# Kernel optimization log

Measured on AMD Instinct MI355X. Metric: run time of the kernel, lower is better.

## Reference

```python
import jax, jax.numpy as jnp
import numpy as np

VOCAB = 50257
EMB = 256
HID = 512
BATCH = 32
SEQ = 512
PAD_ID = 0


def setup_inputs() -> dict:
    key = jax.random.key(0)
    k1, k2, k3, k4, k5, k6 = jax.random.split(key, 6)
    input_ids = jax.random.randint(k1, (BATCH, SEQ), 0, VOCAB, dtype=jnp.int32)
    attention_mask = jax.random.randint(k2, (BATCH, SEQ), 0, 2, dtype=jnp.int32)
    # learned params
    embed_table = jax.random.normal(k3, (VOCAB, EMB), dtype=jnp.float32) * 0.02
    Wx = jax.random.normal(k4, (EMB, HID), dtype=jnp.float32) / np.sqrt(EMB)
    Wh = jax.random.normal(k5, (HID, HID), dtype=jnp.float32) / np.sqrt(HID)
    b = jnp.zeros((HID,), dtype=jnp.float32)
    return {"input_ids": input_ids, "attention_mask": attention_mask,
            "embed_table": embed_table, "Wx": Wx, "Wh": Wh, "b": b}


def reference(input_ids, attention_mask, embed_table, Wx, Wh, b):
    # Embedding lookup: [B, S, E]
    emb = embed_table[input_ids]
    # time-major for scan: [S, B, E] and [S, B]
    xs = jnp.swapaxes(emb, 0, 1)
    ms = jnp.swapaxes(attention_mask, 0, 1)
    h0 = jnp.zeros((emb.shape[0], Wh.shape[0]), dtype=emb.dtype)

    def step(h, xm):
        x_t, m_t = xm  # [B, E], [B]
        h_new = jnp.tanh(x_t @ Wx + h @ Wh + b)  # Elman RNN cell
        h_next = jnp.where((m_t != PAD_ID)[:, None], h_new, h)
        return h_next, h_next

    final_h, all_h_tmajor = jax.lax.scan(step, h0, (xs, ms))
    all_h = jnp.swapaxes(all_h_tmajor, 0, 1)  # [B, S, H]
    return all_h, final_h
```

## Files before the change

### kernel.cpp

```cpp
#include <hip/hip_runtime.h>

#define VOCAB 50257
#define EMB 256
#define HID 512
#define BATCH 32
#define SEQ 512

typedef _Float16 h2 __attribute__((ext_vector_type(2)));
typedef unsigned int u32;

#if __has_builtin(__builtin_amdgcn_fdot2)
#define FDOT2(a, b, c) __builtin_amdgcn_fdot2((a), (b), (c), false)
#else
static __device__ __forceinline__ float FDOT2(h2 a, h2 b, float c) {
    return c + (float)a.x * (float)b.x + (float)a.y * (float)b.y;
}
#endif

#define LBAR() do {                                            \
    asm volatile("s_waitcnt lgkmcnt(0)" ::: "memory");         \
    __builtin_amdgcn_s_barrier();                              \
    asm volatile("" ::: "memory");                             \
} while (0)

static __device__ __forceinline__ h2 mk2(float a, float b) {
    h2 r; r.x = (_Float16)a; r.y = (_Float16)b; return r;
}
static __device__ __forceinline__ u32 pk_rtn(float a, float b) {
    return __builtin_bit_cast(u32, mk2(a, b));
}
static __device__ __forceinline__ h2 as_h2(u32 v) {
    return __builtin_bit_cast(h2, v);
}

__global__ __launch_bounds__(256) void xprec_kernel(
    const int* __restrict__ ids, const float* __restrict__ emb,
    const float* __restrict__ Wx, const float* __restrict__ bias,
    float* __restrict__ allh)
{
    __shared__ float embL[32][EMB];
    const int tid  = threadIdx.x;
    const int tok0 = blockIdx.x * 32;

    {
        const int t    = tid >> 3;
        const int part = tid & 7;
        const int id   = ids[tok0 + t];
        const float4* src = (const float4*)(emb + (size_t)id * EMB + part * 32);
        float4* dst = (float4*)(&embL[t][part * 32]);
#pragma unroll
        for (int k = 0; k < 8; ++k) dst[k] = src[k];
    }
    __syncthreads();

    const int j0 = tid * 2;
    float2 acc[32];
    const float2 bv = *(const float2*)(bias + j0);
#pragma unroll
    for (int t = 0; t < 32; ++t) acc[t] = bv;

    for (int e = 0; e < EMB; e += 4) {
        const float2 w0 = *(const float2*)(Wx + (size_t)(e + 0) * HID + j0);
        const float2 w1 = *(const float2*)(Wx + (size_t)(e + 1) * HID + j0);
        const float2 w2 = *(const float2*)(Wx + (size_t)(e + 2) * HID + j0);
        const float2 w3 = *(const float2*)(Wx + (size_t)(e + 3) * HID + j0);
#pragma unroll
        for (int t = 0; t < 32; ++t) {
            const float4 ev = *(const float4*)(&embL[t][e]);
            acc[t].x += ev.x * w0.x + ev.y * w1.x + ev.z * w2.x + ev.w * w3.x;
            acc[t].y += ev.x * w0.y + ev.y * w1.y + ev.z * w2.y + ev.w * w3.y;
        }
    }

#pragma unroll
    for (int t = 0; t < 32; ++t) {
        *(float2*)(allh + (size_t)(tok0 + t) * HID + j0) = acc[t];
    }
}

__global__ __launch_bounds__(512, 2) void rnn_local_kernel(
    const int* __restrict__ mask, const float* __restrict__ Wh,
    float* __restrict__ allh, float* __restrict__ finalh)
{
    __shared__ uint4 wl[2][8][512];
    __shared__ float zp[8][8][64];
    __shared__ int   mlist[SEQ];
    __shared__ int   nmL;

    const int tid = threadIdx.x;
    const int b   = blockIdx.x;
    const int c   = tid & 63;
    const int p   = tid >> 6;

    int* maskL = (int*)zp;
    maskL[tid] = mask[b * SEQ + tid];
    __syncthreads();
    if (tid == 0) {
        int n = 0;
        for (int t = 0; t < SEQ; ++t) if (maskL[t]) mlist[n++] = t;
        nmL = n;
    }

    const float* wb = Wh + (size_t)(64 * p) * HID + c;
    h2 wv0[32], wv1[32], wv2[32], wv3[32], wv4[32], wv5[32];
#pragma unroll
    for (int i = 0; i < 32; ++i) {
        const float* r0 = wb + (size_t)(2 * i) * HID;
        const float* r1 = r0 + HID;
        wv0[i] = mk2(r0[0 * 64], r1[0 * 64]);
        wv1[i] = mk2(r0[1 * 64], r1[1 * 64]);
        wv2[i] = mk2(r0[2 * 64], r1[2 * 64]);
        wv3[i] = mk2(r0[3 * 64], r1[3 * 64]);
        wv4[i] = mk2(r0[4 * 64], r1[4 * 64]);
        wv5[i] = mk2(r0[5 * 64], r1[5 * 64]);
    }
#pragma unroll
    for (int blk = 0; blk < 8; ++blk) {
        uint4 v6, v7;
        u32* v6p = (u32*)&v6; u32* v7p = (u32*)&v7;
#pragma unroll
        for (int e = 0; e < 4; ++e) {
            const float* r0 = wb + (size_t)(blk * 8 + 2 * e) * HID;
            const float* r1 = r0 + HID;
            v6p[e] = pk_rtn(r0[6 * 64], r1[6 * 64]);
            v7p[e] = pk_rtn(r0[7 * 64], r1[7 * 64]);
        }
        wl[0][blk][tid] = v6;
        wl[1][blk][tid] = v7;
    }
    __syncthreads();
    const int nm = nmL;

    float* arow = allh + (size_t)b * SEQ * HID;

    {
        const int end0 = nm ? mlist[0] : SEQ;
        for (int t = 0; t < end0; ++t) arow[(size_t)t * HID + tid] = 0.f;
    }

    u32   pku  = 0u;
    float hreg = 0.f;
    float xnext = 0.f;
    if (nm) xnext = arow[(size_t)mlist[0] * HID + tid];

    for (int it = 0; it < nm; ++it) {
        const int t    = mlist[it];
        const int tend = (it + 1 < nm) ? mlist[it + 1] : SEQ;
        const float x  = xnext;
        if (it + 1 < nm)
            xnext = arow[(size_t)mlist[it + 1] * HID + tid];

        float a0 = 0.f, a1 = 0.f, a2 = 0.f, a3 = 0.f;
        float a4 = 0.f, a5 = 0.f, a6 = 0.f, a7 = 0.f;
#pragma unroll
        for (int blk = 0; blk < 8; ++blk) {
            const uint4 w6 = wl[0][blk][tid];
            const uint4 w7 = wl[1][blk][tid];
            const u32* w6p = (const u32*)&w6;
            const u32* w7p = (const u32*)&w7;
#pragma unroll
            for (int e = 0; e < 4; ++e) {
                const int i = blk * 4 + e;
                const u32 hu = (u32)__builtin_amdgcn_readlane((int)pku, 2 * i);
                const h2  hv = as_h2(hu);
                a0 = FDOT2(wv0[i], hv, a0);
                a1 = FDOT2(wv1[i], hv, a1);
                a2 = FDOT2(wv2[i], hv, a2);
                a3 = FDOT2(wv3[i], hv, a3);
                a4 = FDOT2(wv4[i], hv, a4);
                a5 = FDOT2(wv5[i], hv, a5);
                a6 = FDOT2(as_h2(w6p[e]), hv, a6);
                a7 = FDOT2(as_h2(w7p[e]), hv, a7);
            }
        }
        zp[p][0][c] = a0; zp[p][1][c] = a1; zp[p][2][c] = a2; zp[p][3][c] = a3;
        zp[p][4][c] = a4; zp[p][5][c] = a5; zp[p][6][c] = a6; zp[p][7][c] = a7;
        LBAR();

        const float z = zp[0][p][c] + zp[1][p][c] + zp[2][p][c] + zp[3][p][c]
                      + zp[4][p][c] + zp[5][p][c] + zp[6][p][c] + zp[7][p][c];
        const float hn = tanhf(x + z);
        hreg = hn;
        for (int tt = t; tt < tend; ++tt)
            arow[(size_t)tt * HID + tid] = hn;

        const float hpartner = __shfl_xor(hn, 1);
        pku = pk_rtn(hn, hpartner);

        LBAR();
    }
    finalh[b * HID + tid] = hreg;
}

extern "C" void kernel_launch(void* const* d_in, const int* in_sizes, int n_in,
                              void* d_out, int out_size, void* d_ws, size_t ws_size,
                              hipStream_t stream) {
    const int*   ids  = (const int*)d_in[0];
    const int*   msk  = (const int*)d_in[1];
    const float* emb  = (const float*)d_in[2];
    const float* Wx   = (const float*)d_in[3];
    const float* Wh   = (const float*)d_in[4];
    const float* bias = (const float*)d_in[5];

    float* allh   = (float*)d_out;
    float* finalh = (float*)d_out + (size_t)BATCH * SEQ * HID;

    xprec_kernel<<<BATCH * SEQ / 32, 256, 0, stream>>>(ids, emb, Wx, bias, allh);
    rnn_local_kernel<<<BATCH, 512, 0, stream>>>(msk, Wh, allh, finalh);
}
```

Baseline: 685.3 us.

## Double-buffer partial sums to drop second barrier, pack partials to fp16, prefetch LDS weights

```diff
diff --git a/kernel.cpp b/kernel.cpp
--- a/kernel.cpp
+++ b/kernel.cpp
@@ -83,8 +83,8 @@
     float* __restrict__ allh, float* __restrict__ finalh)
 {
     __shared__ uint4 wl[2][8][512];
-    __shared__ float zp[8][8][64];
-    __shared__ int   mlist[SEQ];
+    __shared__ u32   zpp[2][8][4][64];
+    __shared__ unsigned short mlist[SEQ];
     __shared__ int   nmL;
 
     const int tid = threadIdx.x;
@@ -92,12 +92,12 @@
     const int c   = tid & 63;
     const int p   = tid >> 6;
 
-    int* maskL = (int*)zp;
+    int* maskL = (int*)zpp;
     maskL[tid] = mask[b * SEQ + tid];
     __syncthreads();
     if (tid == 0) {
         int n = 0;
-        for (int t = 0; t < SEQ; ++t) if (maskL[t]) mlist[n++] = t;
+        for (int t = 0; t < SEQ; ++t) if (maskL[t]) mlist[n++] = (unsigned short)t;
         nmL = n;
     }
 
@@ -152,12 +152,17 @@
 
         float a0 = 0.f, a1 = 0.f, a2 = 0.f, a3 = 0.f;
         float a4 = 0.f, a5 = 0.f, a6 = 0.f, a7 = 0.f;
+        uint4 w6c = wl[0][0][tid];
+        uint4 w7c = wl[1][0][tid];
 #pragma unroll
         for (int blk = 0; blk < 8; ++blk) {
-            const uint4 w6 = wl[0][blk][tid];
-            const uint4 w7 = wl[1][blk][tid];
-            const u32* w6p = (const u32*)&w6;
-            const u32* w7p = (const u32*)&w7;
+            uint4 w6n, w7n;
+            if (blk < 7) {
+                w6n = wl[0][blk + 1][tid];
+                w7n = wl[1][blk + 1][tid];
+            }
+            const u32* w6p = (const u32*)&w6c;
+            const u32* w7p = (const u32*)&w7c;
 #pragma unroll
             for (int e = 0; e < 4; ++e) {
                 const int i = blk * 4 + e;
@@ -172,13 +177,23 @@
                 a6 = FDOT2(as_h2(w6p[e]), hv, a6);
                 a7 = FDOT2(as_h2(w7p[e]), hv, a7);
             }
-        }
-        zp[p][0][c] = a0; zp[p][1][c] = a1; zp[p][2][c] = a2; zp[p][3][c] = a3;
-        zp[p][4][c] = a4; zp[p][5][c] = a5; zp[p][6][c] = a6; zp[p][7][c] = a7;
+            if (blk < 7) { w6c = w6n; w7c = w7n; }
+        }
+
+        const int par = it & 1;
+        zpp[par][p][0][c] = pk_rtn(a0, a1);
+        zpp[par][p][1][c] = pk_rtn(a2, a3);
+        zpp[par][p][2][c] = pk_rtn(a4, a5);
+        zpp[par][p][3][c] = pk_rtn(a6, a7);
         LBAR();
 
-        const float z = zp[0][p][c] + zp[1][p][c] + zp[2][p][c] + zp[3][p][c]
-                      + zp[4][p][c] + zp[5][p][c] + zp[6][p][c] + zp[7][p][c];
+        const int jj = p >> 1;
+        float z = 0.f;
+#pragma unroll
+        for (int kg = 0; kg < 8; ++kg) {
+            const h2 pr = as_h2(zpp[par][kg][jj][c]);
+            z += (float)((p & 1) ? pr.y : pr.x);
+        }
         const float hn = tanhf(x + z);
         hreg = hn;
         for (int tt = t; tt < tend; ++tt)
@@ -186,8 +201,6 @@
 
         const float hpartner = __shfl_xor(hn, 1);
         pku = pk_rtn(hn, hpartner);
-
-        LBAR();
     }
     finalh[b * HID + tid] = hreg;
 }
```

After: 712.6 us. 1.04x slower.

## Split recurrent matvec over 1024 threads with fp16-packed partial sums

Applied to the files above, without the earlier changes.

```diff
diff --git a/kernel.cpp b/kernel.cpp
--- a/kernel.cpp
+++ b/kernel.cpp
@@ -78,56 +78,54 @@
     }
 }
 
-__global__ __launch_bounds__(512, 2) void rnn_local_kernel(
+__global__ __launch_bounds__(1024, 4) void rnn_local_kernel(
     const int* __restrict__ mask, const float* __restrict__ Wh,
     float* __restrict__ allh, float* __restrict__ finalh)
 {
-    __shared__ uint4 wl[2][8][512];
-    __shared__ float zp[8][8][64];
-    __shared__ int   mlist[SEQ];
+    __shared__ uint4 wl[8][1024];
+    __shared__ u32   zpp[8][2][2][64];
+    __shared__ u32   hbuf[256];
+    __shared__ unsigned short mlist[SEQ];
     __shared__ int   nmL;
 
     const int tid = threadIdx.x;
     const int b   = blockIdx.x;
     const int c   = tid & 63;
     const int p   = tid >> 6;
-
-    int* maskL = (int*)zp;
-    maskL[tid] = mask[b * SEQ + tid];
+    const int kp  = p & 7;
+    const int ch  = p >> 3;
+
+    int* maskL = (int*)zpp;
+    if (tid < SEQ) maskL[tid] = mask[b * SEQ + tid];
     __syncthreads();
     if (tid == 0) {
         int n = 0;
-        for (int t = 0; t < SEQ; ++t) if (maskL[t]) mlist[n++] = t;
+        for (int t = 0; t < SEQ; ++t) if (maskL[t]) mlist[n++] = (unsigned short)t;
         nmL = n;
     }
 
-    const float* wb = Wh + (size_t)(64 * p) * HID + c;
-    h2 wv0[32], wv1[32], wv2[32], wv3[32], wv4[32], wv5[32];
-#pragma unroll
-    for (int i = 0; i < 32; ++i) {
-        const float* r0 = wb + (size_t)(2 * i) * HID;
+    const float* wb = Wh + (size_t)(64 * kp) * HID + (256 * ch + c);
+    h2 wA[32], wB[32], wC[32];
+#pragma unroll 4
+    for (int m = 0; m < 32; ++m) {
+        const float* r0 = wb + (size_t)(2 * m) * HID;
         const float* r1 = r0 + HID;
-        wv0[i] = mk2(r0[0 * 64], r1[0 * 64]);
-        wv1[i] = mk2(r0[1 * 64], r1[1 * 64]);
-        wv2[i] = mk2(r0[2 * 64], r1[2 * 64]);
-        wv3[i] = mk2(r0[3 * 64], r1[3 * 64]);
-        wv4[i] = mk2(r0[4 * 64], r1[4 * 64]);
-        wv5[i] = mk2(r0[5 * 64], r1[5 * 64]);
-    }
-#pragma unroll
-    for (int blk = 0; blk < 8; ++blk) {
-        uint4 v6, v7;
-        u32* v6p = (u32*)&v6; u32* v7p = (u32*)&v7;
+        wA[m] = mk2(r0[0],   r1[0]);
+        wB[m] = mk2(r0[64],  r1[64]);
+        wC[m] = mk2(r0[128], r1[128]);
+    }
+#pragma unroll
+    for (int u = 0; u < 8; ++u) {
+        uint4 v; u32* vp = (u32*)&v;
 #pragma unroll
         for (int e = 0; e < 4; ++e) {
-            const float* r0 = wb + (size_t)(blk * 8 + 2 * e) * HID;
+            const float* r0 = wb + (size_t)(8 * u + 2 * e) * HID;
             const float* r1 = r0 + HID;
-            v6p[e] = pk_rtn(r0[6 * 64], r1[6 * 64]);
-            v7p[e] = pk_rtn(r0[7 * 64], r1[7 * 64]);
-        }
-        wl[0][blk][tid] = v6;
-        wl[1][blk][tid] = v7;
-    }
+            vp[e] = pk_rtn(r0[192], r1[192]);
+        }
+        wl[u][tid] = v;
+    }
+    if (tid < 256) hbuf[tid] = 0u;
     __syncthreads();
     const int nm = nmL;
 
@@ -135,61 +133,60 @@
 
     {
         const int end0 = nm ? mlist[0] : SEQ;
-        for (int t = 0; t < end0; ++t) arow[(size_t)t * HID + tid] = 0.f;
-    }
-
-    u32   pku  = 0u;
-    float hreg = 0.f;
-    float xnext = 0.f;
-    if (nm) xnext = arow[(size_t)mlist[0] * HID + tid];
+        if (tid < 512)
+            for (int t = 0; t < end0; ++t) arow[(size_t)t * HID + tid] = 0.f;
+    }
+
+    float hreg = 0.f, xnext = 0.f;
+    if (nm && tid < 512) xnext = arow[(size_t)mlist[0] * HID + tid];
 
     for (int it = 0; it < nm; ++it) {
         const int t    = mlist[it];
         const int tend = (it + 1 < nm) ? mlist[it + 1] : SEQ;
         const float x  = xnext;
-        if (it + 1 < nm)
+        if (tid < 512 && it + 1 < nm)
             xnext = arow[(size_t)mlist[it + 1] * HID + tid];
 
+        const u32 pku = hbuf[32 * kp + (c & 31)];
+
         float a0 = 0.f, a1 = 0.f, a2 = 0.f, a3 = 0.f;
-        float a4 = 0.f, a5 = 0.f, a6 = 0.f, a7 = 0.f;
-#pragma unroll
-        for (int blk = 0; blk < 8; ++blk) {
-            const uint4 w6 = wl[0][blk][tid];
-            const uint4 w7 = wl[1][blk][tid];
-            const u32* w6p = (const u32*)&w6;
-            const u32* w7p = (const u32*)&w7;
+#pragma unroll
+        for (int u = 0; u < 8; ++u) {
+            const uint4 wt = wl[u][tid];
+            const u32* wp = (const u32*)&wt;
 #pragma unroll
             for (int e = 0; e < 4; ++e) {
-                const int i = blk * 4 + e;
-                const u32 hu = (u32)__builtin_amdgcn_readlane((int)pku, 2 * i);
-                const h2  hv = as_h2(hu);
-                a0 = FDOT2(wv0[i], hv, a0);
-                a1 = FDOT2(wv1[i], hv, a1);
-                a2 = FDOT2(wv2[i], hv, a2);
-                a3 = FDOT2(wv3[i], hv, a3);
-                a4 = FDOT2(wv4[i], hv, a4);
-                a5 = FDOT2(wv5[i], hv, a5);
-                a6 = FDOT2(as_h2(w6p[e]), hv, a6);
-                a7 = FDOT2(as_h2(w7p[e]), hv, a7);
+                const int m = 4 * u + e;
+                const h2 hv = as_h2((u32)__builtin_amdgcn_readlane((int)pku, m));
+                a0 = FDOT2(wA[m], hv, a0);
+                a1 = FDOT2(wB[m], hv, a1);
+                a2 = FDOT2(wC[m], hv, a2);
+                a3 = FDOT2(as_h2(wp[e]), hv, a3);
             }
         }
-        zp[p][0][c] = a0; zp[p][1][c] = a1; zp[p][2][c] = a2; zp[p][3][c] = a3;
-        zp[p][4][c] = a4; zp[p][5][c] = a5; zp[p][6][c] = a6; zp[p][7][c] = a7;
+        zpp[kp][ch][0][c] = pk_rtn(a0, a1);
+        zpp[kp][ch][1][c] = pk_rtn(a2, a3);
         LBAR();
 
-        const float z = zp[0][p][c] + zp[1][p][c] + zp[2][p][c] + zp[3][p][c]
-                      + zp[4][p][c] + zp[5][p][c] + zp[6][p][c] + zp[7][p][c];
-        const float hn = tanhf(x + z);
-        hreg = hn;
-        for (int tt = t; tt < tend; ++tt)
-            arow[(size_t)tt * HID + tid] = hn;
-
-        const float hpartner = __shfl_xor(hn, 1);
-        pku = pk_rtn(hn, hpartner);
-
+        if (tid < 512) {
+            const int q  = tid >> 6;
+            const int qh = q >> 2, qe = (q >> 1) & 1, qs = q & 1;
+            float z = 0.f;
+#pragma unroll
+            for (int kg = 0; kg < 8; ++kg) {
+                const h2 pr = as_h2(zpp[kg][qh][qe][c]);
+                z += (float)(qs ? pr.y : pr.x);
+            }
+            const float hn = tanhf(x + z);
+            hreg = hn;
+            for (int tt = t; tt < tend; ++tt)
+                arow[(size_t)tt * HID + tid] = hn;
+            const float hp = __shfl_xor(hn, 1);
+            if ((tid & 1) == 0) hbuf[tid >> 1] = pk_rtn(hn, hp);
+        }
         LBAR();
     }
-    finalh[b * HID + tid] = hreg;
+    if (tid < 512) finalh[b * HID + tid] = hreg;
 }
 
 extern "C" void kernel_launch(void* const* d_in, const int* in_sizes, int n_in,
@@ -206,5 +203,5 @@
     float* finalh = (float*)d_out + (size_t)BATCH * SEQ * HID;
 
     xprec_kernel<<<BATCH * SEQ / 32, 256, 0, stream>>>(ids, emb, Wx, bias, allh);
-    rnn_local_kernel<<<BATCH, 512, 0, stream>>>(msk, Wh, allh, finalh);
-}
+    rnn_local_kernel<<<BATCH, 1024, 0, stream>>>(msk, Wh, allh, finalh);
+}
```

Result: slower. 1.145 ms (+67.1%).
